# Kernel tuning notes

Hardware: AMD Instinct MI355X
Metric: run time of the kernel (lower is better)

The kernel has to match this reference:

```python
import jax, jax.numpy as jnp
import numpy as np

B, S, H, F, E, K = 4, 4096, 1024, 4096, 8, 2
LN_EPS = 1e-5


def setup_inputs() -> dict:
    key = jax.random.key(0)
    kx, kr, k1, k2 = jax.random.split(key, 4)
    x = jax.random.normal(kx, (B, S, H), dtype=jnp.float32)
    gamma = jnp.ones((H,), jnp.float32)
    beta = jnp.zeros((H,), jnp.float32)
    Wr = jax.random.normal(kr, (H, E), jnp.float32) * 0.02
    br = jnp.zeros((E,), jnp.float32)
    W1 = jax.random.normal(k1, (E, H, F), jnp.float32) * (1.0 / np.sqrt(H))
    b1 = jnp.zeros((E, F), jnp.float32)
    W2 = jax.random.normal(k2, (E, F, H), jnp.float32) * (1.0 / np.sqrt(F))
    b2 = jnp.zeros((E, H), jnp.float32)
    return {"x": x, "gamma": gamma, "beta": beta, "Wr": Wr, "br": br,
            "W1": W1, "b1": b1, "W2": W2, "b2": b2}


def reference(x, gamma, beta, Wr, br, W1, b1, W2, b2):
    residual = x
    # LayerNorm (biased variance, torch default eps)
    mu = jnp.mean(x, axis=-1, keepdims=True)
    var = jnp.var(x, axis=-1, keepdims=True)
    xn = (x - mu) * jax.lax.rsqrt(var + LN_EPS) * gamma + beta

    # Router: softmax over expert logits, then top-k
    probs = jax.nn.softmax(xn @ Wr + br, axis=-1)          # [B,S,E]
    scores, idx = jax.lax.top_k(probs, K)                   # [B,S,K]

    # Dense per-expert MLP on the full (unmasked) normalized input.
    # Original computes expert_i(x * mask_i); since mask is {0,1}, per token this
    # equals expert_i(x) when selected and expert_i(0) = relu(b1_i)@W2_i + b2_i
    # (a per-expert constant) when not selected. The original accumulates
    # scores * expert_i(x*mask_i) over ALL experts, so zero-input bias terms of
    # every other expert also contribute, which we reproduce exactly.
    def expert_fn(w):
        W1_e, b1_e, W2_e, b2_e = w
        return jax.nn.relu(xn @ W1_e + b1_e) @ W2_e + b2_e   # [B,S,H]

    full = jax.lax.map(expert_fn, (W1, b1, W2, b2))          # [E,B,S,H]
    full = jnp.moveaxis(full, 0, 2)                           # [B,S,E,H]

    c = jnp.einsum('ef,efh->eh', jax.nn.relu(b1), W2) + b2   # expert_i(0), [E,H]
    c_total = c.sum(axis=0)                                   # [H]

    sel_full = jnp.take_along_axis(full, idx[..., None], axis=2)  # [B,S,K,H]
    c_sel = c[idx]                                                 # [B,S,K,H]

    # sum_k scores_k * ( expert_sel(x) + sum_{i != sel} expert_i(0) )
    output = jnp.sum(scores[..., None] * (sel_full - c_sel + c_total), axis=2)
    return residual + output
```

## Files before the change

kernel.cpp:

```cpp
#include <hip/hip_runtime.h>

#define T_TOKENS 16384
#define HDIM 1024
#define FDIM 4096
#define NEXP 8
#define TM 128
#define PAIR_MAX 33792
#define MAX_RT 264

typedef _Float16 f16;
typedef _Float16 f16x8 __attribute__((ext_vector_type(8)));
typedef _Float16 f16x4 __attribute__((ext_vector_type(4)));
typedef float f32x4 __attribute__((ext_vector_type(4)));

__device__ __forceinline__ void gload_lds16(const void* g, void* l) {
    __builtin_amdgcn_global_load_lds(
        (const __attribute__((address_space(1))) unsigned int*)g,
        (__attribute__((address_space(3))) unsigned int*)l, 16, 0, 0);
}

__global__ void __launch_bounds__(256) transpose_kernel(
    const float* __restrict__ W, f16* __restrict__ WT, int R, int C)
{
    const int e = blockIdx.x;
    const int r0 = blockIdx.y * 32, c0 = blockIdx.z * 32;
    __shared__ float tile[32][33];
    const int tid = threadIdx.x;
    const int rr = tid >> 3, cc = (tid & 7) * 4;
    float4 v = *(const float4*)(W + ((size_t)e * R + r0 + rr) * C + c0 + cc);
    tile[rr][cc + 0] = v.x; tile[rr][cc + 1] = v.y;
    tile[rr][cc + 2] = v.z; tile[rr][cc + 3] = v.w;
    __syncthreads();
    f16x4 hv;
    hv[0] = (f16)tile[cc + 0][rr];
    hv[1] = (f16)tile[cc + 1][rr];
    hv[2] = (f16)tile[cc + 2][rr];
    hv[3] = (f16)tile[cc + 3][rr];
    *(f16x4*)(WT + ((size_t)e * C + c0 + rr) * R + r0 + cc) = hv;
}

__global__ void __launch_bounds__(256) router_kernel(
    const float* __restrict__ x, const float* __restrict__ gamma,
    const float* __restrict__ beta, const float* __restrict__ Wr,
    const float* __restrict__ br,
    f16* __restrict__ xnh, float* __restrict__ scores, int* __restrict__ sidx,
    float* __restrict__ ssum, int* __restrict__ counts)
{
    const int t = blockIdx.x;
    const int tid = threadIdx.x;
    const int lane = tid & 63, wid = tid >> 6;

    float4 v = ((const float4*)(x + (size_t)t * HDIM))[tid];
    float s = v.x + v.y + v.z + v.w;
    float q = v.x * v.x + v.y * v.y + v.z * v.z + v.w * v.w;
#pragma unroll
    for (int o = 32; o > 0; o >>= 1) { s += __shfl_down(s, o); q += __shfl_down(q, o); }

    __shared__ float red[8];
    __shared__ float stat[2];
    if (lane == 0) { red[wid] = s; red[4 + wid] = q; }
    __syncthreads();
    if (tid == 0) {
        float S = red[0] + red[1] + red[2] + red[3];
        float Q = red[4] + red[5] + red[6] + red[7];
        float mu = S * (1.0f / HDIM);
        float var = Q * (1.0f / HDIM) - mu * mu;
        stat[0] = mu; stat[1] = rsqrtf(var + 1e-5f);
    }
    __syncthreads();
    const float mu = stat[0], rstd = stat[1];
    float4 gv = ((const float4*)gamma)[tid];
    float4 bv = ((const float4*)beta)[tid];
    float xn[4];
    xn[0] = (v.x - mu) * rstd * gv.x + bv.x;
    xn[1] = (v.y - mu) * rstd * gv.y + bv.y;
    xn[2] = (v.z - mu) * rstd * gv.z + bv.z;
    xn[3] = (v.w - mu) * rstd * gv.w + bv.w;
    f16x4 hv;
    hv[0] = (f16)xn[0]; hv[1] = (f16)xn[1]; hv[2] = (f16)xn[2]; hv[3] = (f16)xn[3];
    *(f16x4*)(xnh + (size_t)t * HDIM + tid * 4) = hv;

    float lg[8] = {0, 0, 0, 0, 0, 0, 0, 0};
#pragma unroll
    for (int j = 0; j < 4; ++j) {
        const float4* wr = (const float4*)(Wr + (size_t)(tid * 4 + j) * NEXP);
        float4 w0 = wr[0], w1 = wr[1];
        lg[0] += xn[j] * w0.x; lg[1] += xn[j] * w0.y;
        lg[2] += xn[j] * w0.z; lg[3] += xn[j] * w0.w;
        lg[4] += xn[j] * w1.x; lg[5] += xn[j] * w1.y;
        lg[6] += xn[j] * w1.z; lg[7] += xn[j] * w1.w;
    }
#pragma unroll
    for (int o = 32; o > 0; o >>= 1) {
#pragma unroll
        for (int e = 0; e < 8; ++e) lg[e] += __shfl_down(lg[e], o);
    }
    __shared__ float lred[4][8];
    if (lane == 0) {
#pragma unroll
        for (int e = 0; e < 8; ++e) lred[wid][e] = lg[e];
    }
    __syncthreads();
    if (tid == 0) {
        float L[8], m = -1e30f;
        for (int e = 0; e < 8; ++e) {
            L[e] = lred[0][e] + lred[1][e] + lred[2][e] + lred[3][e] + br[e];
            m = fmaxf(m, L[e]);
        }
        float p[8], Z = 0.f;
        for (int e = 0; e < 8; ++e) { p[e] = expf(L[e] - m); Z += p[e]; }
        float invZ = 1.f / Z;
        float best = -1.f, sec = -1.f; int be = 0, se = 0;
        for (int e = 0; e < 8; ++e) {
            float pe = p[e] * invZ;
            if (pe > best) { sec = best; se = be; best = pe; be = e; }
            else if (pe > sec) { sec = pe; se = e; }
        }
        scores[t * 2] = best; scores[t * 2 + 1] = sec;
        sidx[t * 2] = be; sidx[t * 2 + 1] = se;
        ssum[t] = best + sec;
        atomicAdd(&counts[be], 1);
        atomicAdd(&counts[se], 1);
    }
}

__global__ void offsets_kernel(const int* __restrict__ counts, int* __restrict__ bases,
                               int* __restrict__ cursor, int* __restrict__ tile_e,
                               int* __restrict__ tile_row0, int* __restrict__ ntiles)
{
    if (threadIdx.x == 0) {
        int cur = 0, rt = 0;
        for (int e = 0; e < NEXP; ++e) {
            bases[e] = cur; cursor[e] = 0;
            int c = counts[e];
            int nt = (c + TM - 1) / TM;
            for (int i = 0; i < nt; ++i) { tile_e[rt] = e; tile_row0[rt] = cur + i * TM; rt++; }
            cur += nt * TM;
        }
        *ntiles = rt;
    }
}

__global__ void __launch_bounds__(256) scatter_kernel(
    const int* __restrict__ sidx, const float* __restrict__ scores,
    const int* __restrict__ bases, int* __restrict__ cursor,
    int* __restrict__ pair_token, float* __restrict__ pair_score)
{
    int t = blockIdx.x * 256 + threadIdx.x;
#pragma unroll
    for (int k = 0; k < 2; ++k) {
        int e = sidx[t * 2 + k];
        int slot = atomicAdd(&cursor[e], 1);
        int p = bases[e] + slot;
        pair_token[p] = t;
        pair_score[p] = scores[t * 2 + k];
    }
}

__global__ void __launch_bounds__(256) ctotal_kernel(
    const float* __restrict__ b1, const float* __restrict__ W2,
    const float* __restrict__ b2, float* __restrict__ c_total)
{
    const int e = blockIdx.x, ch = blockIdx.y;
    const int tid = threadIdx.x;
    const int h0 = tid * 4;
    float a0 = 0, a1 = 0, a2 = 0, a3 = 0;
    for (int f = ch * 256; f < ch * 256 + 256; ++f) {
        float a = fmaxf(b1[e * FDIM + f], 0.f);
        if (a != 0.f) {
            float4 w = *(const float4*)(W2 + ((size_t)e * FDIM + f) * HDIM + h0);
            a0 += a * w.x; a1 += a * w.y; a2 += a * w.z; a3 += a * w.w;
        }
    }
    if (ch == 0) {
        float4 b2v = *(const float4*)(b2 + e * HDIM + h0);
        a0 += b2v.x; a1 += b2v.y; a2 += b2v.z; a3 += b2v.w;
    }
    atomicAdd(&c_total[h0 + 0], a0);
    atomicAdd(&c_total[h0 + 1], a1);
    atomicAdd(&c_total[h0 + 2], a2);
    atomicAdd(&c_total[h0 + 3], a3);
}

__global__ void __launch_bounds__(256) init_kernel(
    const float* __restrict__ x, const float* __restrict__ ssum,
    const float* __restrict__ c_total, float* __restrict__ out)
{
    const int t = blockIdx.x, tid = threadIdx.x;
    float sv = ssum[t];
    float4 xv = ((const float4*)(x + (size_t)t * HDIM))[tid];
    float4 cv = ((const float4*)c_total)[tid];
    float4 o = {xv.x + sv * cv.x, xv.y + sv * cv.y, xv.z + sv * cv.z, xv.w + sv * cv.w};
    ((float4*)(out + (size_t)t * HDIM))[tid] = o;
}

__global__ void __launch_bounds__(256, 2) gemm1_kernel(
    const f16* __restrict__ xnh, const f16* __restrict__ W1T,
    const float* __restrict__ b1, const int* __restrict__ pair_token,
    const int* __restrict__ tile_e, const int* __restrict__ tile_row0,
    const int* __restrict__ ntiles, f16* __restrict__ g)
{
    const int rt = blockIdx.x;
    if (rt >= *ntiles) return;
    const int e = tile_e[rt];
    const int row0 = tile_row0[rt];
    const int n0 = blockIdx.y * 128;
    const int tid = threadIdx.x;
    const int wave = tid >> 6, lane = tid & 63;
    const int l15 = lane & 15, lk = lane >> 4;
    const int wm = wave >> 1, wn = wave & 1;

    __shared__ __align__(16) f16 As[128 * 64];
    __shared__ __align__(16) f16 Bs[128 * 64];

    const f16* asrc[4];
#pragma unroll
    for (int it = 0; it < 4; ++it) {
        int i = it * 256 + tid;
        int tok = pair_token[row0 + (i >> 3)];
        if (tok < 0) tok = 0;
        asrc[it] = xnh + (size_t)tok * HDIM + (i & 7) * 8;
    }
    const f16* bbase = W1T + ((size_t)e * FDIM + n0) * HDIM;

    f32x4 acc[4][4];
    const f32x4 vzero = {0.f, 0.f, 0.f, 0.f};
#pragma unroll
    for (int a0 = 0; a0 < 4; ++a0)
#pragma unroll
        for (int b0 = 0; b0 < 4; ++b0) acc[a0][b0] = vzero;

    for (int k0 = 0; k0 < HDIM; k0 += 64) {
#pragma unroll
        for (int it = 0; it < 4; ++it) {
            int i = it * 256 + tid;
            gload_lds16(asrc[it] + k0, &As[(size_t)(i & ~63) * 8]);
            gload_lds16(bbase + (size_t)(i >> 3) * HDIM + (i & 7) * 8 + k0,
                        &Bs[(size_t)(i & ~63) * 8]);
        }
        __syncthreads();
#pragma unroll
        for (int ks = 0; ks < 64; ks += 32) {
            f16x8 af[4], bf[4];
#pragma unroll
            for (int fm = 0; fm < 4; ++fm)
                af[fm] = *(const f16x8*)&As[(wm * 64 + fm * 16 + l15) * 64 + ks + lk * 8];
#pragma unroll
            for (int fn = 0; fn < 4; ++fn)
                bf[fn] = *(const f16x8*)&Bs[(wn * 64 + fn * 16 + l15) * 64 + ks + lk * 8];
#pragma unroll
            for (int fm = 0; fm < 4; ++fm)
#pragma unroll
                for (int fn = 0; fn < 4; ++fn)
                    acc[fm][fn] = __builtin_amdgcn_mfma_f32_16x16x32_f16(
                        af[fm], bf[fn], acc[fm][fn], 0, 0, 0);
        }
        __syncthreads();
    }

#pragma unroll
    for (int fn = 0; fn < 4; ++fn) {
        int n = n0 + wn * 64 + fn * 16 + l15;
        float b1v = b1[e * FDIM + n];
        float rb = fmaxf(b1v, 0.f);
#pragma unroll
        for (int fm = 0; fm < 4; ++fm) {
#pragma unroll
            for (int r = 0; r < 4; ++r) {
                int mrow = wm * 64 + fm * 16 + lk * 4 + r;
                float z = acc[fm][fn][r] + b1v;
                g[(size_t)(row0 + mrow) * FDIM + n] = (f16)(fmaxf(z, 0.f) - rb);
            }
        }
    }
}

__global__ void __launch_bounds__(256, 2) gemm2_kernel(
    const f16* __restrict__ g, const f16* __restrict__ W2T,
    const int* __restrict__ pair_token, const float* __restrict__ pair_score,
    const int* __restrict__ tile_e, const int* __restrict__ tile_row0,
    const int* __restrict__ ntiles, float* __restrict__ out)
{
    const int rt = blockIdx.x;
    if (rt >= *ntiles) return;
    const int e = tile_e[rt];
    const int row0 = tile_row0[rt];
    const int n0 = blockIdx.y * 128;
    const int tid = threadIdx.x;
    const int wave = tid >> 6, lane = tid & 63;
    const int l15 = lane & 15, lk = lane >> 4;
    const int wm = wave >> 1, wn = wave & 1;

    __shared__ __align__(16) f16 As[128 * 64];
    __shared__ __align__(16) f16 Bs[128 * 64];

    const f16* bbase = W2T + ((size_t)e * HDIM + n0) * FDIM;

    f32x4 acc[4][4];
    const f32x4 vzero = {0.f, 0.f, 0.f, 0.f};
#pragma unroll
    for (int a0 = 0; a0 < 4; ++a0)
#pragma unroll
        for (int b0 = 0; b0 < 4; ++b0) acc[a0][b0] = vzero;

    for (int k0 = 0; k0 < FDIM; k0 += 64) {
#pragma unroll
        for (int it = 0; it < 4; ++it) {
            int i = it * 256 + tid;
            gload_lds16(g + (size_t)(row0 + (i >> 3)) * FDIM + (i & 7) * 8 + k0,
                        &As[(size_t)(i & ~63) * 8]);
            gload_lds16(bbase + (size_t)(i >> 3) * FDIM + (i & 7) * 8 + k0,
                        &Bs[(size_t)(i & ~63) * 8]);
        }
        __syncthreads();
#pragma unroll
        for (int ks = 0; ks < 64; ks += 32) {
            f16x8 af[4], bf[4];
#pragma unroll
            for (int fm = 0; fm < 4; ++fm)
                af[fm] = *(const f16x8*)&As[(wm * 64 + fm * 16 + l15) * 64 + ks + lk * 8];
#pragma unroll
            for (int fn = 0; fn < 4; ++fn)
                bf[fn] = *(const f16x8*)&Bs[(wn * 64 + fn * 16 + l15) * 64 + ks + lk * 8];
#pragma unroll
            for (int fm = 0; fm < 4; ++fm)
#pragma unroll
                for (int fn = 0; fn < 4; ++fn)
                    acc[fm][fn] = __builtin_amdgcn_mfma_f32_16x16x32_f16(
                        af[fm], bf[fn], acc[fm][fn], 0, 0, 0);
        }
        __syncthreads();
    }

#pragma unroll
    for (int fn = 0; fn < 4; ++fn) {
        int n = n0 + wn * 64 + fn * 16 + l15;
#pragma unroll
        for (int fm = 0; fm < 4; ++fm) {
#pragma unroll
            for (int r = 0; r < 4; ++r) {
                int prow = row0 + wm * 64 + fm * 16 + lk * 4 + r;
                int tok = pair_token[prow];
                if (tok >= 0) {
                    float sc = pair_score[prow];
                    atomicAdd(out + (size_t)tok * HDIM + n, sc * acc[fm][fn][r]);
                }
            }
        }
    }
}

extern "C" void kernel_launch(void* const* d_in, const int* in_sizes, int n_in,
                              void* d_out, int out_size, void* d_ws, size_t ws_size,
                              hipStream_t stream)
{
    const float* x     = (const float*)d_in[0];
    const float* gamma = (const float*)d_in[1];
    const float* beta  = (const float*)d_in[2];
    const float* Wr    = (const float*)d_in[3];
    const float* br    = (const float*)d_in[4];
    const float* W1    = (const float*)d_in[5];
    const float* b1    = (const float*)d_in[6];
    const float* W2    = (const float*)d_in[7];
    const float* b2    = (const float*)d_in[8];
    float* out = (float*)d_out;
    (void)in_sizes; (void)n_in; (void)out_size; (void)ws_size;

    char* ws = (char*)d_ws;
    size_t off = 0;
    auto carve = [&](size_t bytes) {
        char* p = ws + off;
        off += (bytes + 255) & ~(size_t)255;
        return p;
    };
    f16*   xnh        = (f16*)carve((size_t)T_TOKENS * HDIM * 2);
    f16*   w1t        = (f16*)carve((size_t)NEXP * FDIM * HDIM * 2);
    f16*   w2t        = (f16*)carve((size_t)NEXP * HDIM * FDIM * 2);
    f16*   gbuf       = (f16*)carve((size_t)PAIR_MAX * FDIM * 2);
    int*   pair_token = (int*)carve((size_t)PAIR_MAX * 4);
    float* pair_score = (float*)carve((size_t)PAIR_MAX * 4);
    float* scores     = (float*)carve((size_t)T_TOKENS * 2 * 4);
    int*   sidx       = (int*)carve((size_t)T_TOKENS * 2 * 4);
    float* ssum       = (float*)carve((size_t)T_TOKENS * 4);
    float* c_total    = (float*)carve((size_t)HDIM * 4);
    int*   counts     = (int*)carve(NEXP * 4);
    int*   cursor     = (int*)carve(NEXP * 4);
    int*   bases      = (int*)carve(NEXP * 4);
    int*   ntiles     = (int*)carve(4);
    int*   tile_e     = (int*)carve(MAX_RT * 4);
    int*   tile_row0  = (int*)carve(MAX_RT * 4);

    hipMemsetAsync(counts, 0, NEXP * 4, stream);
    hipMemsetAsync(c_total, 0, HDIM * 4, stream);
    hipMemsetAsync(pair_token, 0xFF, (size_t)PAIR_MAX * 4, stream);

    transpose_kernel<<<dim3(NEXP, HDIM / 32, FDIM / 32), 256, 0, stream>>>(W1, w1t, HDIM, FDIM);
    transpose_kernel<<<dim3(NEXP, FDIM / 32, HDIM / 32), 256, 0, stream>>>(W2, w2t, FDIM, HDIM);
    router_kernel<<<T_TOKENS, 256, 0, stream>>>(x, gamma, beta, Wr, br, xnh, scores, sidx, ssum, counts);
    offsets_kernel<<<1, 64, 0, stream>>>(counts, bases, cursor, tile_e, tile_row0, ntiles);
    scatter_kernel<<<T_TOKENS / 256, 256, 0, stream>>>(sidx, scores, bases, cursor, pair_token, pair_score);
    ctotal_kernel<<<dim3(NEXP, FDIM / 256), 256, 0, stream>>>(b1, W2, b2, c_total);
    init_kernel<<<T_TOKENS, 256, 0, stream>>>(x, ssum, c_total, out);
    gemm1_kernel<<<dim3(MAX_RT, FDIM / 128), 256, 0, stream>>>(
        xnh, w1t, b1, pair_token, tile_e, tile_row0, ntiles, gbuf);
    gemm2_kernel<<<dim3(MAX_RT, HDIM / 128), 256, 0, stream>>>(
        gbuf, w2t, pair_token, pair_score, tile_e, tile_row0, ntiles, out);
}
```

Baseline: 1.889 ms.

## XOR-swizzle LDS tiles in expert GEMMs and linearize grid with N-tiles innermost

Loads of A and B tiles into LDS now permute the 16-byte chunks within each 128-byte row by XOR with the row index, and the MFMA fragment reads apply the same swizzle. This is meant to remove the LDS bank conflicts that happen when 16 lanes read the same column offset across consecutive rows. The 2D grid also becomes 1D, with the N-tile index innermost, so consecutive blocks share the same row tile and its gathered A rows, which should improve L2 reuse. The risk is address arithmetic overhead and making sure the swizzle matches between writer and reader.

```diff
diff --git a/kernel.cpp b/kernel.cpp
--- a/kernel.cpp
+++ b/kernel.cpp
@@ -194,32 +194,38 @@
     ((float4*)(out + (size_t)t * HDIM))[tid] = o;
 }
 
+
 __global__ void __launch_bounds__(256, 2) gemm1_kernel(
     const f16* __restrict__ xnh, const f16* __restrict__ W1T,
     const float* __restrict__ b1, const int* __restrict__ pair_token,
     const int* __restrict__ tile_e, const int* __restrict__ tile_row0,
     const int* __restrict__ ntiles, f16* __restrict__ g)
 {
-    const int rt = blockIdx.x;
+    const int idx = blockIdx.x;
+    const int rt = idx >> 5;
     if (rt >= *ntiles) return;
+    const int n0 = (idx & 31) * 128;
     const int e = tile_e[rt];
     const int row0 = tile_row0[rt];
-    const int n0 = blockIdx.y * 128;
     const int tid = threadIdx.x;
     const int wave = tid >> 6, lane = tid & 63;
     const int l15 = lane & 15, lk = lane >> 4;
     const int wm = wave >> 1, wn = wave & 1;
+    const int sx = l15 & 7;
 
     __shared__ __align__(16) f16 As[128 * 64];
     __shared__ __align__(16) f16 Bs[128 * 64];
 
     const f16* asrc[4];
+    int bso[4];
 #pragma unroll
     for (int it = 0; it < 4; ++it) {
         int i = it * 256 + tid;
+        int so = (((i & 7) ^ ((i >> 3) & 7)) << 3);
         int tok = pair_token[row0 + (i >> 3)];
         if (tok < 0) tok = 0;
-        asrc[it] = xnh + (size_t)tok * HDIM + (i & 7) * 8;
+        asrc[it] = xnh + (size_t)tok * HDIM + so;
+        bso[it] = so;
     }
     const f16* bbase = W1T + ((size_t)e * FDIM + n0) * HDIM;
 
@@ -235,19 +241,20 @@
         for (int it = 0; it < 4; ++it) {
             int i = it * 256 + tid;
             gload_lds16(asrc[it] + k0, &As[(size_t)(i & ~63) * 8]);
-            gload_lds16(bbase + (size_t)(i >> 3) * HDIM + (i & 7) * 8 + k0,
+            gload_lds16(bbase + (size_t)(i >> 3) * HDIM + bso[it] + k0,
                         &Bs[(size_t)(i & ~63) * 8]);
         }
         __syncthreads();
 #pragma unroll
         for (int ks = 0; ks < 64; ks += 32) {
+            const int soff = (((lk + (ks >> 3)) ^ sx) << 3);
             f16x8 af[4], bf[4];
 #pragma unroll
             for (int fm = 0; fm < 4; ++fm)
-                af[fm] = *(const f16x8*)&As[(wm * 64 + fm * 16 + l15) * 64 + ks + lk * 8];
+                af[fm] = *(const f16x8*)&As[(wm * 64 + fm * 16 + l15) * 64 + soff];
 #pragma unroll
             for (int fn = 0; fn < 4; ++fn)
-                bf[fn] = *(const f16x8*)&Bs[(wn * 64 + fn * 16 + l15) * 64 + ks + lk * 8];
+                bf[fn] = *(const f16x8*)&Bs[(wn * 64 + fn * 16 + l15) * 64 + soff];
 #pragma unroll
             for (int fm = 0; fm < 4; ++fm)
 #pragma unroll
@@ -281,15 +288,17 @@
     const int* __restrict__ tile_e, const int* __restrict__ tile_row0,
     const int* __restrict__ ntiles, float* __restrict__ out)
 {
-    const int rt = blockIdx.x;
+    const int idx = blockIdx.x;
+    const int rt = idx >> 3;
     if (rt >= *ntiles) return;
+    const int n0 = (idx & 7) * 128;
     const int e = tile_e[rt];
     const int row0 = tile_row0[rt];
-    const int n0 = blockIdx.y * 128;
     const int tid = threadIdx.x;
     const int wave = tid >> 6, lane = tid & 63;
     const int l15 = lane & 15, lk = lane >> 4;
     const int wm = wave >> 1, wn = wave & 1;
+    const int sx = l15 & 7;
 
     __shared__ __align__(16) f16 As[128 * 64];
     __shared__ __align__(16) f16 Bs[128 * 64];
@@ -307,21 +316,23 @@
 #pragma unroll
         for (int it = 0; it < 4; ++it) {
             int i = it * 256 + tid;
-            gload_lds16(g + (size_t)(row0 + (i >> 3)) * FDIM + (i & 7) * 8 + k0,
+            int so = (((i & 7) ^ ((i >> 3) & 7)) << 3);
+            gload_lds16(g + (size_t)(row0 + (i >> 3)) * FDIM + so + k0,
                         &As[(size_t)(i & ~63) * 8]);
-            gload_lds16(bbase + (size_t)(i >> 3) * FDIM + (i & 7) * 8 + k0,
+            gload_lds16(bbase + (size_t)(i >> 3) * FDIM + so + k0,
                         &Bs[(size_t)(i & ~63) * 8]);
         }
         __syncthreads();
 #pragma unroll
         for (int ks = 0; ks < 64; ks += 32) {
+            const int soff = (((lk + (ks >> 3)) ^ sx) << 3);
             f16x8 af[4], bf[4];
 #pragma unroll
             for (int fm = 0; fm < 4; ++fm)
-                af[fm] = *(const f16x8*)&As[(wm * 64 + fm * 16 + l15) * 64 + ks + lk * 8];
+                af[fm] = *(const f16x8*)&As[(wm * 64 + fm * 16 + l15) * 64 + soff];
 #pragma unroll
             for (int fn = 0; fn < 4; ++fn)
-                bf[fn] = *(const f16x8*)&Bs[(wn * 64 + fn * 16 + l15) * 64 + ks + lk * 8];
+                bf[fn] = *(const f16x8*)&Bs[(wn * 64 + fn * 16 + l15) * 64 + soff];
 #pragma unroll
             for (int fm = 0; fm < 4; ++fm)
 #pragma unroll
@@ -401,8 +412,8 @@
     scatter_kernel<<<T_TOKENS / 256, 256, 0, stream>>>(sidx, scores, bases, cursor, pair_token, pair_score);
     ctotal_kernel<<<dim3(NEXP, FDIM / 256), 256, 0, stream>>>(b1, W2, b2, c_total);
     init_kernel<<<T_TOKENS, 256, 0, stream>>>(x, ssum, c_total, out);
-    gemm1_kernel<<<dim3(MAX_RT, FDIM / 128), 256, 0, stream>>>(
+    gemm1_kernel<<<MAX_RT * 32, 256, 0, stream>>>(
         xnh, w1t, b1, pair_token, tile_e, tile_row0, ntiles, gbuf);
-    gemm2_kernel<<<dim3(MAX_RT, HDIM / 128), 256, 0, stream>>>(
+    gemm2_kernel<<<MAX_RT * 8, 256, 0, stream>>>(
         gbuf, w2t, pair_token, pair_score, tile_e, tile_row0, ntiles, out);
 }
```

Result: faster. 1.684 ms (-10.9%).
